# Optimization experiments

Measured on AMD Instinct MI355X. Metric: run time of the kernel, lower is better.

Reference implementation:

```python
import math
from functools import partial

import jax
import jax.numpy as jnp
import numpy as np

DS = 128            # domain_size (cells per side); original used 600
PD = 1.0            # particle diameter d == grid spacing
KN = 500000.0       # normal stiffness
MASS = 1.0
DT = 1e-4
FS = 5              # filter (stencil) size -> 5x5x5 shifts
_ALPHA = -math.log(0.7) / math.pi
_GAMMA = _ALPHA / math.sqrt(_ALPHA ** 2 + 1.0)
ETA = 2.0 * _GAMMA * math.sqrt(KN * MASS)   # damping_coefficient_Eta
EPS = 1e-4          # torch.clamp(dist, 0.0001)
SHAPE = (1, 1, DS, DS, DS)


def setup_inputs() -> dict:
    rng = np.random.default_rng(0)
    occ = np.zeros((DS, DS, DS), np.float32)
    occ[1:-1, 1:-1, 1:-1] = (rng.random((DS - 2,) * 3) < 0.2).astype(np.float32)
    iz, iy, ix = np.meshgrid(np.arange(DS), np.arange(DS), np.arange(DS), indexing="ij")
    jit = lambda: (rng.random((DS,) * 3).astype(np.float32) - 0.5) * 0.4
    # occupied cells store their own coordinate (+jitter) so round(x/d) == cell index
    x = (occ * (ix.astype(np.float32) + jit())).astype(np.float32)
    y = (occ * (iy.astype(np.float32) + jit())).astype(np.float32)
    z = (occ * (iz.astype(np.float32) + jit())).astype(np.float32)
    vel = lambda: (occ * rng.normal(0.0, 0.5, (DS,) * 3)).astype(np.float32)
    asg = lambda a: jnp.asarray(a.reshape(SHAPE))
    return {
        "x_grid": asg(x), "y_grid": asg(y), "z_grid": asg(z),
        "vx_grid": asg(vel()), "vy_grid": asg(vel()), "vz_grid": asg(vel()),
        "mask": asg(occ),
    }


def _contrib(xg, yg, zg, vxg, vyg, vzg, shift):
    """Force contribution from one (i,j,k) stencil shift (torch.roll based)."""
    roll = lambda g: jnp.roll(g, shift, axis=(2, 3, 4))
    dx, dy, dz = xg - roll(xg), yg - roll(yg), zg - roll(zg)
    sq = dx * dx + dy * dy + dz * dz
    dist = jnp.sqrt(sq + 1e-20)  # tiny eps keeps sqrt grad finite at sq==0; value unchanged in fp32
    cd = jnp.maximum(dist, EPS)  # torch.clamp(dist, 0.0001)
    vn = ((vxg - roll(vxg)) * dx + (vyg - roll(vyg)) * dy + (vzg - roll(vzg)) * dz) / cd
    ov = dist < 2.0 * PD
    fx = jnp.where(ov, KN * (dist - 2.0 * PD) * dx / cd + ETA * vn * dx / cd, 0.0)
    fy = jnp.where(ov, KN * (dist - 2.0 * PD) * dy / cd + ETA * vn * dy / cd, 0.0)
    fz = jnp.where(ov, KN * (dist - 2.0 * PD) * dz / cd + ETA * vn * dz / cd, 0.0)
    return fx, fy, fz


def _forward(xg, yg, zg, vxg, vyg, vzg, mask):
    f32 = jnp.float32
    fx = jnp.zeros(SHAPE, f32)
    fy = jnp.zeros(SHAPE, f32)
    fz = jnp.zeros(SHAPE, f32)
    for i in range(FS):
        for j in range(FS):
            for k in range(FS):
                c = jax.checkpoint(partial(_contrib, shift=(k - 2, j - 2, i - 2)))
                dfx, dfy, dfz = c(xg, yg, zg, vxg, vyg, vzg)
                fx, fy, fz = fx + dfx, fy + dfy, fz + dfz
    # boundary overlap forces
    bl = ((xg != 0.0) & (xg < PD)).astype(f32)
    br = (xg > DS - 2.0 * PD).astype(f32)
    bb = ((yg != 0.0) & (yg < PD)).astype(f32)
    bt = (yg > DS - 2.0 * PD).astype(f32)
    bf = ((zg != 0.0) & (zg < PD)).astype(f32)
    bk = (zg > DS - 2.0 * PD).astype(f32)
    fxb = KN * bl * mask * (PD - xg) - KN * br * mask * (xg - DS + 2.0 * PD) - ETA * vxg * bl * mask - ETA * vxg * br * mask
    fyb = KN * bb * mask * (PD - yg) - KN * bt * mask * (yg - DS + 2.0 * PD) - ETA * vyg * bb * mask - ETA * vyg * bt * mask
    fzb = KN * bf * mask * (PD - zg) - KN * bk * mask * (zg - DS + 2.0 * PD) - ETA * vzg * bf * mask - ETA * vzg * bk * mask
    vxn = vxg + DT / MASS * mask * (-0.0 * MASS - fx + fxb)
    vyn = vyg + DT / MASS * mask * (-9.8 * MASS - fy + fyb)
    vzn = vzg + DT / MASS * mask * (-0.0 * MASS - fz + fzb)
    cell = lambda g: jnp.round(g / PD).astype(jnp.int32)
    cx0, cy0, cz0 = cell(xg), cell(yg), cell(zg)
    xn, yn, zn = xg + DT * vxn, yg + DT * vyn, zg + DT * vzn
    cx1, cy1, cz1 = cell(xn), cell(yn), cell(zn)
    # cell-list relocation: flatten to linear indices; invalid (empty) cells -> dump slot D3
    D3 = DS ** 3
    def lin(cz, cy, cx):
        v = (cx != 0) & (cy != 0) & (cz != 0)   # torch filters cell_* != 0
        return jnp.where(v, (cz * DS + cy) * DS + cx, D3).reshape(-1)
    lo = lin(cz0, cy0, cx0)
    ln = lin(cz1, cy1, cx1)
    pad = lambda g: jnp.concatenate([g.reshape(-1), jnp.zeros((1,), g.dtype)])
    unpad = lambda f: f[:D3].reshape(SHAPE)
    def move(g):
        gf = pad(g)
        return unpad(gf.at[lo].set(0.0).at[ln].set(gf[lo]))
    mask_n = unpad(pad(mask).at[lo].set(0.0).at[ln].set(1.0))
    return (move(xn), move(yn), move(zn), move(vxn), move(vyn), move(vzn), mask_n)


def reference(x_grid, y_grid, z_grid, vx_grid, vy_grid, vz_grid, mask):
    return _forward(x_grid, y_grid, z_grid, vx_grid, vy_grid, vz_grid, mask)
```

## Files before the change

kernel.cpp:

```cpp
#include <hip/hip_runtime.h>

#define DSZ   128
#define DMSK  127
#define D3    (DSZ * DSZ * DSZ)

#define KN_F   500000.0f
#define ETA_F  159.535258f
#define DT_F   1e-4f

#define TBX   32
#define TBY   4
#define TBZ   4
#define HALO  2
#define RS    37
#define PS    296
#define SLOTS 2368
#define NT    512

struct OffTabs { int a[36]; int b[48]; int e[44]; };
constexpr OffTabs make_tabs() {
    OffTabs t{}; int na = 0, nb = 0, ne = 0;
    for (int dz = -2; dz <= 2; ++dz)
        for (int dy = -2; dy <= 2; ++dy)
            for (int dx = -2; dx <= 2; ++dx) {
                const int r2 = dz*dz + dy*dy + dx*dx;
                const int off = dz * PS + dy * RS + dx;
                if (r2 <= 4)      t.a[na++] = off;
                else if (r2 <= 6) t.b[nb++] = off;
                else              t.e[ne++] = off;
            }
    while (na < 36) t.a[na++] = 0;
    return t;
}
__constant__ OffTabs g_tabs = make_tabs();

typedef float f4a4 __attribute__((ext_vector_type(4), aligned(4)));

__device__ __forceinline__ unsigned bf16_rne(float f) {
    unsigned u = __float_as_uint(f);
    u += 0x7fffu + ((u >> 16) & 1u);
    return u >> 16;
}
__device__ __forceinline__ unsigned packvv(float vy, float vz) {
    return bf16_rne(vy) | (bf16_rne(vz) << 16);
}
__device__ __forceinline__ float unpk_lo(unsigned w) { return __uint_as_float(w << 16); }
__device__ __forceinline__ float unpk_hi(unsigned w) { return __uint_as_float(w & 0xffff0000u); }

__device__ __forceinline__ void pair_full(
    const float4* __restrict__ lsp, const unsigned* __restrict__ lsv, int n,
    float px, float py, float pz, float vx, float vy, float vz,
    float& fx, float& fy, float& fz)
{
    const float4 q = lsp[n];
    const float ddx = px - q.x, ddy = py - q.y, ddz = pz - q.z;
    const float sq  = fmaf(ddx, ddx, fmaf(ddy, ddy, fmaf(ddz, ddz, 1e-20f)));
    const float rsd = __builtin_amdgcn_rsqf(sq);
    const float dist = sq * rsd;
    const unsigned w = lsv[n];
    const float vn = (fmaf(vx - q.w, ddx, fmaf(vy - unpk_lo(w), ddy, (vz - unpk_hi(w)) * ddz))) * rsd;
    float coef = fmaf(KN_F, dist - 2.0f, ETA_F * vn) * rsd;
    coef = (dist < 2.0f) ? coef : 0.0f;
    fx = fmaf(coef, ddx, fx);
    fy = fmaf(coef, ddy, fy);
    fz = fmaf(coef, ddz, fz);
}

__global__ __launch_bounds__(NT) void dem_tile(
    const float* __restrict__ X, const float* __restrict__ Y, const float* __restrict__ Z,
    const float* __restrict__ VX, const float* __restrict__ VY, const float* __restrict__ VZ,
    float* __restrict__ out)
{
    __shared__ float4 lsp[SLOTS];
    __shared__ unsigned lsv[SLOTS];
    __shared__ unsigned short plist[NT];
    __shared__ int loff[128];
    __shared__ unsigned int pcnt;
    __shared__ int nreloc;
    __shared__ int relocidx[8];
    __shared__ float relocval[8][7];

    const int tid = threadIdx.x;

    const unsigned raw = blockIdx.x;
    const unsigned xcd = raw & 7, loc = raw >> 3;
    const int bx = (int)((loc & 3) * TBX);
    const int by = (int)(((loc >> 2) & 31) * TBY);
    const int bz = (int)((xcd * 4 + (loc >> 7)) * TBZ);

    if (tid == 0) { pcnt = 0; nreloc = 0; }
    if (tid < 36) loff[tid] = g_tabs.a[tid];
    else if (tid < 84) loff[tid] = g_tabs.b[tid - 36];
    else if (tid < 128) loff[tid] = g_tabs.e[tid - 84];

    for (int u = tid; u < 2880; u += NT) {
        if (u < 2048) {
            const int f = u & 3, t = u >> 2, k = t & 7, r = t >> 3;
            const int hz = r >> 3, hy = r & 7;
            const int gz = (bz + hz - HALO) & DMSK;
            const int gy = (by + hy - HALO) & DMSK;
            const float* F = (f == 0) ? X : (f == 1) ? Y : (f == 2) ? Z : VX;
            const f4a4 a = *(const f4a4*)(F + (gz * DSZ + gy) * DSZ + bx + k * 4);
            float* lb = (float*)lsp + (hz * PS + hy * RS + k * 4 + HALO) * 4 + f;
            #pragma unroll
            for (int e = 0; e < 4; ++e) lb[e * 4] = a[e];
        } else if (u < 2560) {
            const int v = u - 2048, k = v & 7, r = v >> 3;
            const int hz = r >> 3, hy = r & 7;
            const int gz = (bz + hz - HALO) & DMSK;
            const int gy = (by + hy - HALO) & DMSK;
            const int gb = (gz * DSZ + gy) * DSZ + bx + k * 4;
            const f4a4 yv = *(const f4a4*)(VY + gb);
            const f4a4 zv = *(const f4a4*)(VZ + gb);
            unsigned* vb = lsv + hz * PS + hy * RS + k * 4 + HALO;
            #pragma unroll
            for (int e = 0; e < 4; ++e) vb[e] = packvv(yv[e], zv[e]);
        } else if (u < 2816) {
            const int w = u - 2560, f = w & 3, r = w >> 2;
            const int hz = r >> 3, hy = r & 7;
            const int gz = (bz + hz - HALO) & DMSK;
            const int gy = (by + hy - HALO) & DMSK;
            const float* F = (f == 0) ? X : (f == 1) ? Y : (f == 2) ? Z : VX;
            const int rowg = (gz * DSZ + gy) * DSZ;
            float* lb = (float*)lsp + (hz * PS + hy * RS) * 4 + f;
            lb[0]      = F[rowg + ((bx - 2) & DMSK)];
            lb[4]      = F[rowg + ((bx - 1) & DMSK)];
            lb[34 * 4] = F[rowg + ((bx + 32) & DMSK)];
            lb[35 * 4] = F[rowg + ((bx + 33) & DMSK)];
        } else {
            const int r = u - 2816;
            const int hz = r >> 3, hy = r & 7;
            const int gz = (bz + hz - HALO) & DMSK;
            const int gy = (by + hy - HALO) & DMSK;
            const int rowg = (gz * DSZ + gy) * DSZ;
            unsigned* vb = lsv + hz * PS + hy * RS;
            const int g0 = rowg + ((bx - 2) & DMSK), g1 = rowg + ((bx - 1) & DMSK);
            const int g2 = rowg + ((bx + 32) & DMSK), g3 = rowg + ((bx + 33) & DMSK);
            vb[0]  = packvv(VY[g0], VZ[g0]);
            vb[1]  = packvv(VY[g1], VZ[g1]);
            vb[34] = packvv(VY[g2], VZ[g2]);
            vb[35] = packvv(VY[g3], VZ[g3]);
        }
    }

    __syncthreads();

    const int tx = tid & 31, ty = (tid >> 5) & 3, tz = tid >> 7;
    const int cg = ((bz + tz) * DSZ + (by + ty)) * DSZ + (bx + tx);
    const int lcc = (tz + HALO) * PS + (ty + HALO) * RS + (tx + HALO);
    const float4 qo = lsp[lcc];
    const unsigned wo = lsv[lcc];
    const bool occ = (qo.x != 0.0f);

    {
        const unsigned long long bmask = __ballot(occ);
        const int lane = tid & 63;
        const unsigned int prefix = (unsigned int)__popcll(bmask & ((1ull << lane) - 1ull));
        unsigned int base = 0;
        if (lane == 0) base = atomicAdd(&pcnt, (unsigned int)__popcll(bmask));
        base = __shfl(base, 0, 64);
        if (occ) plist[base + prefix] = (unsigned short)tid;
    }

    float ev[7];
    if (!occ) {
        const float px = qo.x, py = qo.y, pz = qo.z;
        const float vx = qo.w, vy = unpk_lo(wo), vz = unpk_hi(wo);
        const float xn = px + DT_F * vx, yn = py + DT_F * vy, zn = pz + DT_F * vz;
        const int cx0 = (int)rintf(px), cy0 = (int)rintf(py), cz0 = (int)rintf(pz);
        const int cx1 = (int)rintf(xn), cy1 = (int)rintf(yn), cz1 = (int)rintf(zn);
        const int lo = (cx0 && cy0 && cz0) ? ((cz0 * DSZ + cy0) * DSZ + cx0) : D3;
        const int ln = (cx1 && cy1 && cz1) ? ((cz1 * DSZ + cy1) * DSZ + cx1) : D3;
        const bool zeroed = (lo == cg) && (ln != cg);
        const float mk = (ln == cg) ? 1.0f : 0.0f;
        ev[0] = zeroed ? 0.f : xn; ev[1] = zeroed ? 0.f : yn; ev[2] = zeroed ? 0.f : zn;
        ev[3] = zeroed ? 0.f : vx; ev[4] = zeroed ? 0.f : vy; ev[5] = zeroed ? 0.f : vz;
        ev[6] = mk;
        if (lo != cg && lo < D3) {
            int s = atomicAdd(&nreloc, 1);
            if (s < 8) { relocidx[s] = lo; for (int f = 0; f < 7; ++f) relocval[s][f] = 0.f; }
        }
        if (ln != cg && ln < D3) {
            int s = atomicAdd(&nreloc, 1);
            if (s < 8) {
                relocidx[s] = ln;
                relocval[s][0] = xn; relocval[s][1] = yn; relocval[s][2] = zn;
                relocval[s][3] = vx; relocval[s][4] = vy; relocval[s][5] = vz;
                relocval[s][6] = 1.f;
            }
        }
    }

    __syncthreads();

    const int n = (int)pcnt;
    const int grp = tid >> 2, sub = tid & 3;
    const int npass = (n + 127) >> 7;
    float fa[4], fb[4];
    int fcell[4] = { -1, -1, -1, -1 };

    int offA[9], offB[12];
    #pragma unroll
    for (int t = 0; t < 9; ++t)  offA[t] = loff[t * 4 + sub];
    #pragma unroll
    for (int t = 0; t < 12; ++t) offB[t] = loff[36 + t * 4 + sub];

    for (int pp = 0; pp < npass; ++pp) {
        const int i = pp * 128 + grp;
        if (i >= n) break;
        const int p  = plist[i];
        const int px_ = p & 31, py_ = (p >> 5) & 3, pz_ = p >> 7;
        const int lc = (pz_ + HALO) * PS + (py_ + HALO) * RS + (px_ + HALO);
        const int cpg = ((bz + pz_) * DSZ + (by + py_)) * DSZ + (bx + px_);

        const float4 qc = lsp[lc];
        const unsigned wc = lsv[lc];
        const float px = qc.x, py = qc.y, pz = qc.z;
        const float vx = qc.w, vy = unpk_lo(wc), vz = unpk_hi(wc);
        float fx = 0.f, fy = 0.f, fz = 0.f;

        #pragma unroll
        for (int t = 0; t < 9; ++t)
            pair_full(lsp, lsv, lc + offA[t], px, py, pz, vx, vy, vz, fx, fy, fz);

        #pragma unroll
        for (int t = 0; t < 12; ++t) {
            const int nn = lc + offB[t];
            const float4 q = lsp[nn];
            const float ddx = px - q.x, ddy = py - q.y, ddz = pz - q.z;
            const float sq = fmaf(ddx, ddx, fmaf(ddy, ddy, fmaf(ddz, ddz, 1e-20f)));
            if (sq < 4.0f) {
                const float rsd = __builtin_amdgcn_rsqf(sq);
                const float dist = sq * rsd;
                const unsigned w = lsv[nn];
                const float vn = (fmaf(vx - q.w, ddx, fmaf(vy - unpk_lo(w), ddy, (vz - unpk_hi(w)) * ddz))) * rsd;
                const float coef = fmaf(KN_F, dist - 2.0f, ETA_F * vn) * rsd;
                fx = fmaf(coef, ddx, fx);
                fy = fmaf(coef, ddy, fy);
                fz = fmaf(coef, ddz, fz);
            }
        }

        const float sqo = px*px + py*py + pz*pz;
        if (sqo < 4.0f) {
            for (int t = sub; t < 44; t += 4)
                pair_full(lsp, lsv, lc + loff[84 + t], px, py, pz, vx, vy, vz, fx, fy, fz);
        }

        fx += __shfl_xor(fx, 1); fy += __shfl_xor(fy, 1); fz += __shfl_xor(fz, 1);
        fx += __shfl_xor(fx, 2); fy += __shfl_xor(fy, 2); fz += __shfl_xor(fz, 2);

        const float bl = (px != 0.0f && px < 1.0f)  ? 1.0f : 0.0f;
        const float br = (px > 126.0f)              ? 1.0f : 0.0f;
        const float bb = (py != 0.0f && py < 1.0f)  ? 1.0f : 0.0f;
        const float bt = (py > 126.0f)              ? 1.0f : 0.0f;
        const float bf = (pz != 0.0f && pz < 1.0f)  ? 1.0f : 0.0f;
        const float bk = (pz > 126.0f)              ? 1.0f : 0.0f;
        const float fxb = KN_F * bl * (1.0f - px) - KN_F * br * (px - 126.0f) - ETA_F * vx * (bl + br);
        const float fyb = KN_F * bb * (1.0f - py) - KN_F * bt * (py - 126.0f) - ETA_F * vy * (bb + bt);
        const float fzb = KN_F * bf * (1.0f - pz) - KN_F * bk * (pz - 126.0f) - ETA_F * vz * (bf + bk);

        const float vxn = vx + DT_F * (-fx + fxb);
        const float vyn = vy + DT_F * (-9.8f - fy + fyb);
        const float vzn = vz + DT_F * (-fz + fzb);
        const float xn = px + DT_F * vxn;
        const float yn = py + DT_F * vyn;
        const float zn = pz + DT_F * vzn;

        const int cx0 = (int)rintf(px), cy0 = (int)rintf(py), cz0 = (int)rintf(pz);
        const int cx1 = (int)rintf(xn), cy1 = (int)rintf(yn), cz1 = (int)rintf(zn);
        const int lo = (cx0 && cy0 && cz0) ? ((cz0 * DSZ + cy0) * DSZ + cx0) : D3;
        const int ln = (cx1 && cy1 && cz1) ? ((cz1 * DSZ + cy1) * DSZ + cx1) : D3;

        const bool zeroed = (lo == cpg) && (ln != cpg);
        const float mk = (ln == cpg) ? 1.0f : (zeroed ? 0.0f : 1.0f);
        const float o0 = zeroed ? 0.f : xn,  o1 = zeroed ? 0.f : yn,  o2 = zeroed ? 0.f : zn;
        const float o3 = zeroed ? 0.f : vxn, o4 = zeroed ? 0.f : vyn, o5 = zeroed ? 0.f : vzn;

        fcell[pp] = p;
        fa[pp] = (sub == 0) ? o0 : (sub == 1) ? o1 : (sub == 2) ? o2 : o3;
        fb[pp] = (sub == 0) ? o4 : (sub == 1) ? o5 : mk;

        if (sub == 0) {
            if (lo != cpg && lo < D3) {
                int s = atomicAdd(&nreloc, 1);
                if (s < 8) { relocidx[s] = lo; for (int f = 0; f < 7; ++f) relocval[s][f] = 0.f; }
            }
            if (ln != cpg && ln < D3) {
                int s = atomicAdd(&nreloc, 1);
                if (s < 8) {
                    relocidx[s] = ln;
                    relocval[s][0] = xn;  relocval[s][1] = yn;  relocval[s][2] = zn;
                    relocval[s][3] = vxn; relocval[s][4] = vyn; relocval[s][5] = vzn;
                    relocval[s][6] = 1.f;
                }
            }
        }
    }

    __syncthreads();

    float* res = (float*)lsp;
    if (!occ) {
        #pragma unroll
        for (int f = 0; f < 7; ++f) res[f * 512 + tid] = ev[f];
    }
    #pragma unroll
    for (int pp = 0; pp < 4; ++pp) {
        if (fcell[pp] >= 0) {
            res[sub * 512 + fcell[pp]] = fa[pp];
            if (sub < 3) res[(sub + 4) * 512 + fcell[pp]] = fb[pp];
        }
    }

    __syncthreads();

    for (int u = tid; u < 896; u += NT) {
        const int f = u >> 7, j = u & 127;
        const int cell = 4 * j;
        const int wtx = cell & 31, wty = (cell >> 5) & 3, wtz = cell >> 7;
        const float4 v = *(const float4*)(res + f * 512 + cell);
        *(float4*)(out + f * D3 + ((bz + wtz) * DSZ + (by + wty)) * DSZ + bx + wtx) = v;
    }

    __syncthreads();
    const int nr = nreloc < 8 ? nreloc : 8;
    if (tid < nr) {
        const int idx = relocidx[tid];
        #pragma unroll
        for (int f = 0; f < 7; ++f) out[idx + f * D3] = relocval[tid][f];
    }
}

extern "C" void kernel_launch(void* const* d_in, const int* in_sizes, int n_in,
                              void* d_out, int out_size, void* d_ws, size_t ws_size,
                              hipStream_t stream)
{
    const float* X  = (const float*)d_in[0];
    const float* Y  = (const float*)d_in[1];
    const float* Z  = (const float*)d_in[2];
    const float* VX = (const float*)d_in[3];
    const float* VY = (const float*)d_in[4];
    const float* VZ = (const float*)d_in[5];
    float* out = (float*)d_out;

    dem_tile<<<(D3 / (TBX * TBY * TBZ)), NT, 0, stream>>>(X, Y, Z, VX, VY, VZ, out);
}
```

Baseline: 174.3 us.

## Quantize staged positions to 16-bit fixed point and repack shared-memory layout

Positions are now stored in LDS as 16-bit fixed point (scaled by 512), packed with a bf16 vx into three 32-bit planes instead of a float4 plus a packed velocity word. This cuts the shared-memory footprint and the number of LDS bytes read per neighbour pair, and simplifies the halo staging loop. The cost is extra integer-to-float conversions per pair and reduced position precision. With the large stiffness constant, that precision loss can noticeably perturb forces and output positions. Per-thread offset tables are no longer kept in registers and are re-read from LDS inside the loop.

```diff
diff --git a/kernel.cpp b/kernel.cpp
--- a/kernel.cpp
+++ b/kernel.cpp
@@ -16,6 +16,9 @@
 #define PS    296
 #define SLOTS 2368
 #define NT    512
+
+#define Q512  512.0f
+#define IQ512 0.001953125f
 
 struct OffTabs { int a[36]; int b[48]; int e[44]; };
 constexpr OffTabs make_tabs() {
@@ -36,29 +39,35 @@
 
 typedef float f4a4 __attribute__((ext_vector_type(4), aligned(4)));
 
+__device__ __forceinline__ unsigned q16(float x) {
+    return (unsigned)(int)rintf(x * Q512);
+}
 __device__ __forceinline__ unsigned bf16_rne(float f) {
     unsigned u = __float_as_uint(f);
     u += 0x7fffu + ((u >> 16) & 1u);
     return u >> 16;
 }
-__device__ __forceinline__ unsigned packvv(float vy, float vz) {
-    return bf16_rne(vy) | (bf16_rne(vz) << 16);
-}
 __device__ __forceinline__ float unpk_lo(unsigned w) { return __uint_as_float(w << 16); }
 __device__ __forceinline__ float unpk_hi(unsigned w) { return __uint_as_float(w & 0xffff0000u); }
 
 __device__ __forceinline__ void pair_full(
-    const float4* __restrict__ lsp, const unsigned* __restrict__ lsv, int n,
+    const unsigned* __restrict__ lab, const unsigned* __restrict__ lcd,
+    const unsigned* __restrict__ lvv, int n,
     float px, float py, float pz, float vx, float vy, float vz,
     float& fx, float& fy, float& fz)
 {
-    const float4 q = lsp[n];
-    const float ddx = px - q.x, ddy = py - q.y, ddz = pz - q.z;
+    const unsigned ab = lab[n], cd = lcd[n];
+    const float ddx = fmaf((float)(ab & 0xffffu), -IQ512, px);
+    const float ddy = fmaf((float)(ab >> 16),     -IQ512, py);
+    const float ddz = fmaf((float)(cd & 0xffffu), -IQ512, pz);
     const float sq  = fmaf(ddx, ddx, fmaf(ddy, ddy, fmaf(ddz, ddz, 1e-20f)));
     const float rsd = __builtin_amdgcn_rsqf(sq);
     const float dist = sq * rsd;
-    const unsigned w = lsv[n];
-    const float vn = (fmaf(vx - q.w, ddx, fmaf(vy - unpk_lo(w), ddy, (vz - unpk_hi(w)) * ddz))) * rsd;
+    const unsigned w = lvv[n];
+    const float dvx = vx - __uint_as_float(cd & 0xffff0000u);
+    const float dvy = vy - unpk_lo(w);
+    const float dvz = vz - unpk_hi(w);
+    const float vn = fmaf(dvx, ddx, fmaf(dvy, ddy, dvz * ddz)) * rsd;
     float coef = fmaf(KN_F, dist - 2.0f, ETA_F * vn) * rsd;
     coef = (dist < 2.0f) ? coef : 0.0f;
     fx = fmaf(coef, ddx, fx);
@@ -71,8 +80,7 @@
     const float* __restrict__ VX, const float* __restrict__ VY, const float* __restrict__ VZ,
     float* __restrict__ out)
 {
-    __shared__ float4 lsp[SLOTS];
-    __shared__ unsigned lsv[SLOTS];
+    __shared__ unsigned lsbuf[3 * SLOTS];
     __shared__ unsigned short plist[NT];
     __shared__ int loff[128];
     __shared__ unsigned int pcnt;
@@ -80,6 +88,10 @@
     __shared__ int relocidx[8];
     __shared__ float relocval[8][7];
 
+    unsigned* lab = lsbuf;
+    unsigned* lcd = lsbuf + SLOTS;
+    unsigned* lvv = lsbuf + 2 * SLOTS;
+
     const int tid = threadIdx.x;
 
     const unsigned raw = blockIdx.x;
@@ -93,53 +105,46 @@
     else if (tid < 84) loff[tid] = g_tabs.b[tid - 36];
     else if (tid < 128) loff[tid] = g_tabs.e[tid - 84];
 
-    for (int u = tid; u < 2880; u += NT) {
-        if (u < 2048) {
-            const int f = u & 3, t = u >> 2, k = t & 7, r = t >> 3;
-            const int hz = r >> 3, hy = r & 7;
-            const int gz = (bz + hz - HALO) & DMSK;
-            const int gy = (by + hy - HALO) & DMSK;
-            const float* F = (f == 0) ? X : (f == 1) ? Y : (f == 2) ? Z : VX;
-            const f4a4 a = *(const f4a4*)(F + (gz * DSZ + gy) * DSZ + bx + k * 4);
-            float* lb = (float*)lsp + (hz * PS + hy * RS + k * 4 + HALO) * 4 + f;
-            #pragma unroll
-            for (int e = 0; e < 4; ++e) lb[e * 4] = a[e];
-        } else if (u < 2560) {
-            const int v = u - 2048, k = v & 7, r = v >> 3;
+    for (int u = tid; u < 1728; u += NT) {
+        if (u < 1536) {
+            const int a = u >> 9;
+            const int j = u & 511;
+            const int k = j & 7, r = j >> 3;
             const int hz = r >> 3, hy = r & 7;
             const int gz = (bz + hz - HALO) & DMSK;
             const int gy = (by + hy - HALO) & DMSK;
             const int gb = (gz * DSZ + gy) * DSZ + bx + k * 4;
-            const f4a4 yv = *(const f4a4*)(VY + gb);
-            const f4a4 zv = *(const f4a4*)(VZ + gb);
-            unsigned* vb = lsv + hz * PS + hy * RS + k * 4 + HALO;
+            const float* F0 = (a == 0) ? X : (a == 1) ? Z : VY;
+            const float* F1 = (a == 0) ? Y : (a == 1) ? VX : VZ;
+            const f4a4 p0 = *(const f4a4*)(F0 + gb);
+            const f4a4 p1 = *(const f4a4*)(F1 + gb);
+            unsigned* dst = lsbuf + a * SLOTS + hz * PS + hy * RS + HALO + k * 4;
             #pragma unroll
-            for (int e = 0; e < 4; ++e) vb[e] = packvv(yv[e], zv[e]);
-        } else if (u < 2816) {
-            const int w = u - 2560, f = w & 3, r = w >> 2;
-            const int hz = r >> 3, hy = r & 7;
-            const int gz = (bz + hz - HALO) & DMSK;
-            const int gy = (by + hy - HALO) & DMSK;
-            const float* F = (f == 0) ? X : (f == 1) ? Y : (f == 2) ? Z : VX;
-            const int rowg = (gz * DSZ + gy) * DSZ;
-            float* lb = (float*)lsp + (hz * PS + hy * RS) * 4 + f;
-            lb[0]      = F[rowg + ((bx - 2) & DMSK)];
-            lb[4]      = F[rowg + ((bx - 1) & DMSK)];
-            lb[34 * 4] = F[rowg + ((bx + 32) & DMSK)];
-            lb[35 * 4] = F[rowg + ((bx + 33) & DMSK)];
+            for (int e = 0; e < 4; ++e)
+                dst[e] = (a == 0) ? (q16(p0[e]) | (q16(p1[e]) << 16))
+                       : (a == 1) ? (q16(p0[e]) | (bf16_rne(p1[e]) << 16))
+                                  : (bf16_rne(p0[e]) | (bf16_rne(p1[e]) << 16));
         } else {
-            const int r = u - 2816;
+            const int v = u - 1536;
+            const int a = v >> 6;
+            const int r = v & 63;
             const int hz = r >> 3, hy = r & 7;
             const int gz = (bz + hz - HALO) & DMSK;
             const int gy = (by + hy - HALO) & DMSK;
             const int rowg = (gz * DSZ + gy) * DSZ;
-            unsigned* vb = lsv + hz * PS + hy * RS;
-            const int g0 = rowg + ((bx - 2) & DMSK), g1 = rowg + ((bx - 1) & DMSK);
-            const int g2 = rowg + ((bx + 32) & DMSK), g3 = rowg + ((bx + 33) & DMSK);
-            vb[0]  = packvv(VY[g0], VZ[g0]);
-            vb[1]  = packvv(VY[g1], VZ[g1]);
-            vb[34] = packvv(VY[g2], VZ[g2]);
-            vb[35] = packvv(VY[g3], VZ[g3]);
+            const int gxs[4] = { (bx - 2) & DMSK, (bx - 1) & DMSK,
+                                 (bx + 32) & DMSK, (bx + 33) & DMSK };
+            const int hxs[4] = { 0, 1, 34, 35 };
+            const float* F0 = (a == 0) ? X : (a == 1) ? Z : VY;
+            const float* F1 = (a == 0) ? Y : (a == 1) ? VX : VZ;
+            unsigned* dst = lsbuf + a * SLOTS + hz * PS + hy * RS;
+            #pragma unroll
+            for (int e = 0; e < 4; ++e) {
+                const float f0 = F0[rowg + gxs[e]], f1 = F1[rowg + gxs[e]];
+                dst[hxs[e]] = (a == 0) ? (q16(f0) | (q16(f1) << 16))
+                            : (a == 1) ? (q16(f0) | (bf16_rne(f1) << 16))
+                                       : (bf16_rne(f0) | (bf16_rne(f1) << 16));
+            }
         }
     }
 
@@ -148,9 +153,8 @@
     const int tx = tid & 31, ty = (tid >> 5) & 3, tz = tid >> 7;
     const int cg = ((bz + tz) * DSZ + (by + ty)) * DSZ + (bx + tx);
     const int lcc = (tz + HALO) * PS + (ty + HALO) * RS + (tx + HALO);
-    const float4 qo = lsp[lcc];
-    const unsigned wo = lsv[lcc];
-    const bool occ = (qo.x != 0.0f);
+    const unsigned oab = lab[lcc];
+    const bool occ = ((oab & 0xffffu) != 0u);
 
     {
         const unsigned long long bmask = __ballot(occ);
@@ -162,10 +166,14 @@
         if (occ) plist[base + prefix] = (unsigned short)tid;
     }
 
-    float ev[7];
+    float ev[7] = { 0.f, 0.f, 0.f, 0.f, 0.f, 0.f, 0.f };
     if (!occ) {
-        const float px = qo.x, py = qo.y, pz = qo.z;
-        const float vx = qo.w, vy = unpk_lo(wo), vz = unpk_hi(wo);
+        const unsigned ocd = lcd[lcc], ow = lvv[lcc];
+        const float px = (float)(oab & 0xffffu) * IQ512;
+        const float py = (float)(oab >> 16) * IQ512;
+        const float pz = (float)(ocd & 0xffffu) * IQ512;
+        const float vx = __uint_as_float(ocd & 0xffff0000u);
+        const float vy = unpk_lo(ow), vz = unpk_hi(ow);
         const float xn = px + DT_F * vx, yn = py + DT_F * vy, zn = pz + DT_F * vz;
         const int cx0 = (int)rintf(px), cy0 = (int)rintf(py), cz0 = (int)rintf(pz);
         const int cx1 = (int)rintf(xn), cy1 = (int)rintf(yn), cz1 = (int)rintf(zn);
@@ -196,14 +204,9 @@
     const int n = (int)pcnt;
     const int grp = tid >> 2, sub = tid & 3;
     const int npass = (n + 127) >> 7;
-    float fa[4], fb[4];
+    float fa[4] = { 0.f, 0.f, 0.f, 0.f };
+    float fb[4] = { 0.f, 0.f, 0.f, 0.f };
     int fcell[4] = { -1, -1, -1, -1 };
-
-    int offA[9], offB[12];
-    #pragma unroll
-    for (int t = 0; t < 9; ++t)  offA[t] = loff[t * 4 + sub];
-    #pragma unroll
-    for (int t = 0; t < 12; ++t) offB[t] = loff[36 + t * 4 + sub];
 
     for (int pp = 0; pp < npass; ++pp) {
         const int i = pp * 128 + grp;
@@ -213,27 +216,33 @@
         const int lc = (pz_ + HALO) * PS + (py_ + HALO) * RS + (px_ + HALO);
         const int cpg = ((bz + pz_) * DSZ + (by + py_)) * DSZ + (bx + px_);
 
-        const float4 qc = lsp[lc];
-        const unsigned wc = lsv[lc];
-        const float px = qc.x, py = qc.y, pz = qc.z;
-        const float vx = qc.w, vy = unpk_lo(wc), vz = unpk_hi(wc);
+        const unsigned cab = lab[lc], ccd = lcd[lc], cw = lvv[lc];
+        const float px = (float)(cab & 0xffffu) * IQ512;
+        const float py = (float)(cab >> 16) * IQ512;
+        const float pz = (float)(ccd & 0xffffu) * IQ512;
+        const float vx = __uint_as_float(ccd & 0xffff0000u);
+        const float vy = unpk_lo(cw), vz = unpk_hi(cw);
         float fx = 0.f, fy = 0.f, fz = 0.f;
 
         #pragma unroll
         for (int t = 0; t < 9; ++t)
-            pair_full(lsp, lsv, lc + offA[t], px, py, pz, vx, vy, vz, fx, fy, fz);
+            pair_full(lab, lcd, lvv, lc + loff[t * 4 + sub], px, py, pz, vx, vy, vz, fx, fy, fz);
 
         #pragma unroll
         for (int t = 0; t < 12; ++t) {
-            const int nn = lc + offB[t];
-            const float4 q = lsp[nn];
-            const float ddx = px - q.x, ddy = py - q.y, ddz = pz - q.z;
+            const int nn = lc + loff[36 + t * 4 + sub];
+            const unsigned ab = lab[nn], cd = lcd[nn];
+            const float ddx = fmaf((float)(ab & 0xffffu), -IQ512, px);
+            const float ddy = fmaf((float)(ab >> 16),     -IQ512, py);
+            const float ddz = fmaf((float)(cd & 0xffffu), -IQ512, pz);
             const float sq = fmaf(ddx, ddx, fmaf(ddy, ddy, fmaf(ddz, ddz, 1e-20f)));
             if (sq < 4.0f) {
                 const float rsd = __builtin_amdgcn_rsqf(sq);
                 const float dist = sq * rsd;
-                const unsigned w = lsv[nn];
-                const float vn = (fmaf(vx - q.w, ddx, fmaf(vy - unpk_lo(w), ddy, (vz - unpk_hi(w)) * ddz))) * rsd;
+                const unsigned w = lvv[nn];
+                const float dvx = vx - __uint_as_float(cd & 0xffff0000u);
+                const float vn = fmaf(dvx, ddx,
+                                   fmaf(vy - unpk_lo(w), ddy, (vz - unpk_hi(w)) * ddz)) * rsd;
                 const float coef = fmaf(KN_F, dist - 2.0f, ETA_F * vn) * rsd;
                 fx = fmaf(coef, ddx, fx);
                 fy = fmaf(coef, ddy, fy);
@@ -241,10 +250,10 @@
             }
         }
 
-        const float sqo = px*px + py*py + pz*pz;
+        const float sqo = fmaf(px, px, fmaf(py, py, pz * pz));
         if (sqo < 4.0f) {
             for (int t = sub; t < 44; t += 4)
-                pair_full(lsp, lsv, lc + loff[84 + t], px, py, pz, vx, vy, vz, fx, fy, fz);
+                pair_full(lab, lcd, lvv, lc + loff[84 + t], px, py, pz, vx, vy, vz, fx, fy, fz);
         }
 
         fx += __shfl_xor(fx, 1); fy += __shfl_xor(fy, 1); fz += __shfl_xor(fz, 1);
@@ -300,7 +309,7 @@
 
     __syncthreads();
 
-    float* res = (float*)lsp;
+    float* res = (float*)lsbuf;
     if (!occ) {
         #pragma unroll
         for (int f = 0; f < 7; ++f) res[f * 512 + tid] = ev[f];
```

After: 176.8 us. About the same (+1.5%).
